# Kernel optimization log

Hardware: AMD Instinct MI355X
Metric: run time of the kernel (lower is better)

## Reference

```python
import jax, jax.numpy as jnp
import numpy as np

B, C, H, W = 512, 128, 7, 7
P = 21            # patch_size
DIL = 2           # dilation_patch
PAD = DIL * (P // 2)  # 20: max displacement in pixels


def setup_inputs() -> dict:
    key = jax.random.key(0)
    k1, k2, k3, k4 = jax.random.split(key, 4)
    patch1 = jax.random.normal(k1, (B, C, H, W), jnp.float32)
    patch2 = jax.random.normal(k2, (B, C, H, W), jnp.float32)
    feat = P * P * H * W  # 21609
    w_bbox = jax.random.normal(k3, (4, feat), jnp.float32) * (1.0 / np.sqrt(feat))
    b_bbox = jax.random.normal(k4, (4,), jnp.float32) * 0.01
    return {"patch1": patch1, "patch2": patch2, "w_bbox": w_bbox, "b_bbox": b_bbox}


def _correlation(patch1, patch2):
    """SpatialCorrelationSampler(patch_size=21, dilation_patch=2, kernel_size=1).

    out[b,p,q,i,j] = sum_c patch1[b,c,i,j] * patch2[b,c, i + 2*(p-10), j + 2*(q-10)]
    with zero padding for out-of-bounds displacements. Output: [B, 21, 21, 7, 7].
    """
    padded = jnp.pad(patch2, ((0, 0), (0, 0), (PAD, PAD), (PAD, PAD)))  # [B,C,47,47]
    # Outer product over spatial positions, contracted over channels:
    # T[b,i,j,u,v] = sum_c patch1[b,c,i,j] * padded[b,c,u,v]
    T = jnp.einsum('bcij,bcuv->bijuv', patch1, padded)  # [B,7,7,47,47]
    # Gather the displaced entries: u = 2p + i, v = 2q + j
    Pp, Qq, Ii, Jj = jnp.meshgrid(jnp.arange(P), jnp.arange(P),
                                  jnp.arange(H), jnp.arange(W), indexing='ij')
    corr = T[:, Ii, Jj, DIL * Pp + Ii, DIL * Qq + Jj]  # [B,21,21,7,7]
    return corr


def reference(patch1, patch2, w_bbox, b_bbox):
    corr = _correlation(patch1, patch2)           # [B,21,21,7,7]
    x = corr.reshape(corr.shape[0], -1)           # flatten(start_dim=1)
    return x @ w_bbox.T + b_bbox                  # [B,4]
```

## Files before the change

kernel.cpp:

```cpp
#include <hip/hip_runtime.h>

#define NB    512
#define FEAT  21609
#define CHW   6272
#define NV4   1568
#define PLANE 5120

__constant__ unsigned char c_pa[25] = {0,4,14,18,28,32,42,46,  1,5,17,29,33,45,
                                       7,11,21,25,35,39,       8,12,24,36,40};
__constant__ unsigned char c_pb[25] = {2,6,16,20,30,34,44,48,  3,15,19,31,43,47,
                                       9,13,23,27,37,41,       10,22,26,38,255};

__device__ __forceinline__ unsigned short f2bf(float x) {
    unsigned u = __float_as_uint(x);
    u += 0x7fffu + ((u >> 16) & 1u);
    return (unsigned short)(u >> 16);
}
__device__ __forceinline__ float bf2f(unsigned short h) {
    return __uint_as_float((unsigned)h << 16);
}

__global__ __launch_bounds__(256) void corr_head_kernel(
    const float* __restrict__ patch1,
    const float* __restrict__ patch2,
    const float* __restrict__ w_bbox,
    const float* __restrict__ b_bbox,
    float* __restrict__ out)
{
    __shared__ __align__(16) unsigned short s1b[CHW];
    __shared__ __align__(16) float          s2p[2 * PLANE];
    __shared__ __align__(16) ushort4        s_wq[784];
    __shared__ float s_red[16];

    const int tid = threadIdx.x;
    const int b   = blockIdx.x;

    for (int n = tid; n < 1024; n += 256) {
        int jp = n >> 9, c = (n >> 2) & 127, u = n & 3;
        s2p[jp * PLANE + c * 40 + 28 + u] = 0.f;
    }
    for (int n = tid; n < 896; n += 256) {
        int c = n / 7, i2 = n - 7 * c;
        s2p[PLANE + c * 40 + i2 * 4 + 3] = 0.f;
    }

    const float4* g1 = (const float4*)(patch1 + (size_t)b * CHW);
    for (int t = tid; t < NV4; t += 256) {
        float4 v = g1[t];
        ((ushort4*)s1b)[t] = make_ushort4(f2bf(v.x), f2bf(v.y), f2bf(v.z), f2bf(v.w));
    }

    const float4* g2 = (const float4*)(patch2 + (size_t)b * CHW);
    for (int t = tid; t < NV4; t += 256) {
        float4 v = g2[t];
        int e = t * 4;
        int c = e / 49;
        int r = e - 49 * c;
        #pragma unroll
        for (int k = 0; k < 4; ++k) {
            int i2 = (r * 37) >> 8;
            int j2 = r - 7 * i2;
            s2p[(j2 & 1) * PLANE + c * 40 + i2 * 4 + (j2 >> 1)] = (&v.x)[k];
            if (++r == 49) { r = 0; ++c; }
        }
    }

    for (int n = tid; n < 784; n += 256) {
        int ij = n % 49, tu = n / 49;
        int t = tu >> 2, u = tu & 3;
        int i = ij / 7, j = ij - 7 * i;
        int i2 = (i & 1) + 2 * t, j2 = (j & 1) + 2 * u;
        ushort4 wq = make_ushort4(0, 0, 0, 0);
        if (i2 < 7 && j2 < 7) {
            int p = 10 + ((i2 - i) >> 1);
            int q = 10 + ((j2 - j) >> 1);
            int f = ((p * 21 + q) * 7 + i) * 7 + j;
            wq = make_ushort4(f2bf(w_bbox[f]), f2bf(w_bbox[FEAT + f]),
                              f2bf(w_bbox[2 * FEAT + f]), f2bf(w_bbox[3 * FEAT + f]));
        }
        s_wq[n] = wq;
    }
    __syncthreads();

    float a0 = 0.f, a1 = 0.f, a2 = 0.f, a3 = 0.f;
    if (tid < 200) {
        const int slot = tid >> 3, cs = tid & 7;
        const int ija  = c_pa[slot];
        const int ijbr = c_pb[slot];
        const bool has_b = (ijbr < 49);
        const int ijb  = has_b ? ijbr : ija;
        const int i = ija / 7, j = ija - 7 * i;
        const float* base2 = s2p + (j & 1) * PLANE + (i & 1) * 4;

        float da[4][4], db[4][4];
        #pragma unroll
        for (int t = 0; t < 4; ++t)
            #pragma unroll
            for (int u = 0; u < 4; ++u) { da[t][u] = 0.f; db[t][u] = 0.f; }

        #pragma unroll 2
        for (int cc = 0; cc < 16; ++cc) {
            int c = cs + 8 * cc;
            float f1a = bf2f(s1b[c * 49 + ija]);
            float f1b = bf2f(s1b[c * 49 + ijb]);
            const float* bc = base2 + c * 40;
            #pragma unroll
            for (int t = 0; t < 4; ++t) {
                float4 f2 = *(const float4*)(bc + 8 * t);
                da[t][0] = fmaf(f1a, f2.x, da[t][0]);
                da[t][1] = fmaf(f1a, f2.y, da[t][1]);
                da[t][2] = fmaf(f1a, f2.z, da[t][2]);
                da[t][3] = fmaf(f1a, f2.w, da[t][3]);
                db[t][0] = fmaf(f1b, f2.x, db[t][0]);
                db[t][1] = fmaf(f1b, f2.y, db[t][1]);
                db[t][2] = fmaf(f1b, f2.z, db[t][2]);
                db[t][3] = fmaf(f1b, f2.w, db[t][3]);
            }
        }

        #pragma unroll
        for (int t = 0; t < 4; ++t)
            #pragma unroll
            for (int u = 0; u < 4; ++u) {
                ushort4 wq = s_wq[(4 * t + u) * 49 + ija];
                float d = da[t][u];
                a0 = fmaf(d, bf2f(wq.x), a0);
                a1 = fmaf(d, bf2f(wq.y), a1);
                a2 = fmaf(d, bf2f(wq.z), a2);
                a3 = fmaf(d, bf2f(wq.w), a3);
            }
        if (has_b) {
            #pragma unroll
            for (int t = 0; t < 4; ++t)
                #pragma unroll
                for (int u = 0; u < 4; ++u) {
                    ushort4 wq = s_wq[(4 * t + u) * 49 + ijb];
                    float d = db[t][u];
                    a0 = fmaf(d, bf2f(wq.x), a0);
                    a1 = fmaf(d, bf2f(wq.y), a1);
                    a2 = fmaf(d, bf2f(wq.z), a2);
                    a3 = fmaf(d, bf2f(wq.w), a3);
                }
        }
    }

    for (int off = 32; off > 0; off >>= 1) {
        a0 += __shfl_down(a0, off, 64);
        a1 += __shfl_down(a1, off, 64);
        a2 += __shfl_down(a2, off, 64);
        a3 += __shfl_down(a3, off, 64);
    }
    if ((tid & 63) == 0) {
        int w = tid >> 6;
        s_red[w * 4 + 0] = a0;
        s_red[w * 4 + 1] = a1;
        s_red[w * 4 + 2] = a2;
        s_red[w * 4 + 3] = a3;
    }
    __syncthreads();
    if (tid < 4) {
        float r = s_red[tid] + s_red[4 + tid] + s_red[8 + tid] + s_red[12 + tid];
        out[b * 4 + tid] = r + b_bbox[tid];
    }
}

extern "C" void kernel_launch(void* const* d_in, const int* in_sizes, int n_in,
                              void* d_out, int out_size, void* d_ws, size_t ws_size,
                              hipStream_t stream) {
    const float* patch1 = (const float*)d_in[0];
    const float* patch2 = (const float*)d_in[1];
    const float* w_bbox = (const float*)d_in[2];
    const float* b_bbox = (const float*)d_in[3];
    float* out = (float*)d_out;
    corr_head_kernel<<<dim3(NB), dim3(256), 0, stream>>>(patch1, patch2, w_bbox, b_bbox, out);
}
```

Baseline: 80.27 us.

## Split channels across four blocks per batch with atomic reduction and precomputed weight table

The main kernel now splits each batch's 128 channels across four blocks of 32 channels. Each block writes its partial result to the output with atomicAdd, which raises the grid from 512 to 2048 blocks and cuts shared memory per block. A small setup kernel fills the output with the bias and gathers the 784 needed weight entries into an fp32 table in workspace, so the per-block weight gather and bf16 conversion go away. Global loads are issued up front to overlap their latency. The cost is an extra launch, float atomics that make the summation order nondeterministic, and four times the weight-table loads.

Measured after the change: 81.45 us. No clear change (+1.5%).

```diff
diff --git a/kernel.cpp b/kernel.cpp
--- a/kernel.cpp
+++ b/kernel.cpp
@@ -3,8 +3,11 @@
 #define NB    512
 #define FEAT  21609
 #define CHW   6272
-#define NV4   1568
-#define PLANE 5120
+#define PARTS 4
+#define CPB   32
+#define CELL  1568
+#define V4B   392
+#define PLANE 1280
 
 __constant__ unsigned char c_pa[25] = {0,4,14,18,28,32,42,46,  1,5,17,29,33,45,
                                        7,11,21,25,35,39,       8,12,24,36,40};
@@ -20,65 +23,103 @@
     return __uint_as_float((unsigned)h << 16);
 }
 
-__global__ __launch_bounds__(256) void corr_head_kernel(
-    const float* __restrict__ patch1,
-    const float* __restrict__ patch2,
+__global__ __launch_bounds__(256) void setup_kernel(
     const float* __restrict__ w_bbox,
     const float* __restrict__ b_bbox,
-    float* __restrict__ out)
+    float* __restrict__ out,
+    float4* __restrict__ wtab)
 {
-    __shared__ __align__(16) unsigned short s1b[CHW];
-    __shared__ __align__(16) float          s2p[2 * PLANE];
-    __shared__ __align__(16) ushort4        s_wq[784];
-    __shared__ float s_red[16];
-
-    const int tid = threadIdx.x;
-    const int b   = blockIdx.x;
-
-    for (int n = tid; n < 1024; n += 256) {
-        int jp = n >> 9, c = (n >> 2) & 127, u = n & 3;
-        s2p[jp * PLANE + c * 40 + 28 + u] = 0.f;
-    }
-    for (int n = tid; n < 896; n += 256) {
-        int c = n / 7, i2 = n - 7 * c;
-        s2p[PLANE + c * 40 + i2 * 4 + 3] = 0.f;
-    }
-
-    const float4* g1 = (const float4*)(patch1 + (size_t)b * CHW);
-    for (int t = tid; t < NV4; t += 256) {
-        float4 v = g1[t];
-        ((ushort4*)s1b)[t] = make_ushort4(f2bf(v.x), f2bf(v.y), f2bf(v.z), f2bf(v.w));
-    }
-
-    const float4* g2 = (const float4*)(patch2 + (size_t)b * CHW);
-    for (int t = tid; t < NV4; t += 256) {
-        float4 v = g2[t];
-        int e = t * 4;
-        int c = e / 49;
-        int r = e - 49 * c;
-        #pragma unroll
-        for (int k = 0; k < 4; ++k) {
-            int i2 = (r * 37) >> 8;
-            int j2 = r - 7 * i2;
-            s2p[(j2 & 1) * PLANE + c * 40 + i2 * 4 + (j2 >> 1)] = (&v.x)[k];
-            if (++r == 49) { r = 0; ++c; }
-        }
-    }
-
-    for (int n = tid; n < 784; n += 256) {
+    const int tid = threadIdx.x, bid = blockIdx.x;
+    int k = bid * 256 + tid;
+    if (k < 4 * NB) out[k] = b_bbox[k & 3];
+
+    int n = bid * 98 + tid;
+    if (tid < 98 && n < 784) {
         int ij = n % 49, tu = n / 49;
         int t = tu >> 2, u = tu & 3;
         int i = ij / 7, j = ij - 7 * i;
         int i2 = (i & 1) + 2 * t, j2 = (j & 1) + 2 * u;
-        ushort4 wq = make_ushort4(0, 0, 0, 0);
+        float4 wq = make_float4(0.f, 0.f, 0.f, 0.f);
         if (i2 < 7 && j2 < 7) {
             int p = 10 + ((i2 - i) >> 1);
             int q = 10 + ((j2 - j) >> 1);
             int f = ((p * 21 + q) * 7 + i) * 7 + j;
-            wq = make_ushort4(f2bf(w_bbox[f]), f2bf(w_bbox[FEAT + f]),
-                              f2bf(w_bbox[2 * FEAT + f]), f2bf(w_bbox[3 * FEAT + f]));
-        }
-        s_wq[n] = wq;
+            wq = make_float4(w_bbox[f], w_bbox[FEAT + f],
+                             w_bbox[2 * FEAT + f], w_bbox[3 * FEAT + f]);
+        }
+        wtab[n] = wq;
+    }
+}
+
+__global__ __launch_bounds__(256, 4) void corr_head_kernel(
+    const float* __restrict__ patch1,
+    const float* __restrict__ patch2,
+    const float4* __restrict__ wtab,
+    float* __restrict__ out)
+{
+    __shared__ __align__(16) unsigned short s1b[CELL];
+    __shared__ __align__(16) float          s2p[2 * PLANE];
+    __shared__ __align__(16) float4         s_wf[784];
+    __shared__ float s_red[16];
+
+    const int tid  = threadIdx.x;
+    const int b    = blockIdx.x >> 2;
+    const int part = blockIdx.x & 3;
+
+    const float4* g1 = (const float4*)(patch1 + (size_t)b * CHW + part * CELL);
+    const float4* g2 = (const float4*)(patch2 + (size_t)b * CHW + part * CELL);
+
+    float4 A0 = g1[tid];
+    float4 B0 = g2[tid];
+    float4 A1, B1;
+    const bool tail = tid < (V4B - 256);
+    if (tail) { A1 = g1[tid + 256]; B1 = g2[tid + 256]; }
+    float4 W0 = wtab[tid];
+    float4 W1 = wtab[tid + 256];
+    float4 W2 = wtab[tid + 512];
+    float4 W3;
+    const bool wtail = tid < (784 - 768);
+    if (wtail) W3 = wtab[tid + 768];
+
+    { int jp = tid >> 7, c = (tid >> 2) & 31, u = tid & 3;
+      s2p[jp * PLANE + c * 40 + 28 + u] = 0.f; }
+    if (tid < 224) {
+        int c = tid / 7, i2 = tid - 7 * c;
+        s2p[PLANE + c * 40 + i2 * 4 + 3] = 0.f;
+    }
+
+    s_wf[tid]       = W0;
+    s_wf[tid + 256] = W1;
+    s_wf[tid + 512] = W2;
+    if (wtail) s_wf[tid + 768] = W3;
+
+    ((ushort4*)s1b)[tid] = make_ushort4(f2bf(A0.x), f2bf(A0.y), f2bf(A0.z), f2bf(A0.w));
+    if (tail)
+        ((ushort4*)s1b)[tid + 256] = make_ushort4(f2bf(A1.x), f2bf(A1.y), f2bf(A1.z), f2bf(A1.w));
+
+    {
+        int e = tid * 4;
+        int c = e / 49;
+        int r = e - 49 * c;
+        #pragma unroll
+        for (int k2 = 0; k2 < 4; ++k2) {
+            int i2 = (r * 37) >> 8;
+            int j2 = r - 7 * i2;
+            s2p[(j2 & 1) * PLANE + c * 40 + i2 * 4 + (j2 >> 1)] = (&B0.x)[k2];
+            if (++r == 49) { r = 0; ++c; }
+        }
+    }
+    if (tail) {
+        int e = (tid + 256) * 4;
+        int c = e / 49;
+        int r = e - 49 * c;
+        #pragma unroll
+        for (int k2 = 0; k2 < 4; ++k2) {
+            int i2 = (r * 37) >> 8;
+            int j2 = r - 7 * i2;
+            s2p[(j2 & 1) * PLANE + c * 40 + i2 * 4 + (j2 >> 1)] = (&B1.x)[k2];
+            if (++r == 49) { r = 0; ++c; }
+        }
     }
     __syncthreads();
 
@@ -98,8 +139,8 @@
             #pragma unroll
             for (int u = 0; u < 4; ++u) { da[t][u] = 0.f; db[t][u] = 0.f; }
 
-        #pragma unroll 2
-        for (int cc = 0; cc < 16; ++cc) {
+        #pragma unroll
+        for (int cc = 0; cc < 4; ++cc) {
             int c = cs + 8 * cc;
             float f1a = bf2f(s1b[c * 49 + ija]);
             float f1b = bf2f(s1b[c * 49 + ijb]);
@@ -122,24 +163,24 @@
         for (int t = 0; t < 4; ++t)
             #pragma unroll
             for (int u = 0; u < 4; ++u) {
-                ushort4 wq = s_wq[(4 * t + u) * 49 + ija];
+                float4 wq = s_wf[(4 * t + u) * 49 + ija];
                 float d = da[t][u];
-                a0 = fmaf(d, bf2f(wq.x), a0);
-                a1 = fmaf(d, bf2f(wq.y), a1);
-                a2 = fmaf(d, bf2f(wq.z), a2);
-                a3 = fmaf(d, bf2f(wq.w), a3);
+                a0 = fmaf(d, wq.x, a0);
+                a1 = fmaf(d, wq.y, a1);
+                a2 = fmaf(d, wq.z, a2);
+                a3 = fmaf(d, wq.w, a3);
             }
         if (has_b) {
             #pragma unroll
             for (int t = 0; t < 4; ++t)
                 #pragma unroll
                 for (int u = 0; u < 4; ++u) {
-                    ushort4 wq = s_wq[(4 * t + u) * 49 + ijb];
+                    float4 wq = s_wf[(4 * t + u) * 49 + ijb];
                     float d = db[t][u];
-                    a0 = fmaf(d, bf2f(wq.x), a0);
-                    a1 = fmaf(d, bf2f(wq.y), a1);
-                    a2 = fmaf(d, bf2f(wq.z), a2);
-                    a3 = fmaf(d, bf2f(wq.w), a3);
+                    a0 = fmaf(d, wq.x, a0);
+                    a1 = fmaf(d, wq.y, a1);
+                    a2 = fmaf(d, wq.z, a2);
+                    a3 = fmaf(d, wq.w, a3);
                 }
         }
     }
@@ -160,7 +201,7 @@
     __syncthreads();
     if (tid < 4) {
         float r = s_red[tid] + s_red[4 + tid] + s_red[8 + tid] + s_red[12 + tid];
-        out[b * 4 + tid] = r + b_bbox[tid];
+        atomicAdd(&out[b * 4 + tid], r);
     }
 }
 
@@ -172,5 +213,8 @@
     const float* w_bbox = (const float*)d_in[2];
     const float* b_bbox = (const float*)d_in[3];
     float* out = (float*)d_out;
-    corr_head_kernel<<<dim3(NB), dim3(256), 0, stream>>>(patch1, patch2, w_bbox, b_bbox, out);
-}
+    float4* wtab = (float4*)d_ws;
+
+    setup_kernel<<<dim3(8), dim3(256), 0, stream>>>(w_bbox, b_bbox, out, wtab);
+    corr_head_kernel<<<dim3(NB * PARTS), dim3(256), 0, stream>>>(patch1, patch2, wtab, out);
+}
```
